# Optimization experiments

Measured on AMD Instinct MI355X. Metric: run time of the kernel, lower is better.

Reference implementation:

```python
import jax, jax.numpy as jnp
import numpy as np

N_NODES = 100000
N_EDGES = 3200000
IN_DIM = 128
OUT_DIM = 128


def setup_inputs() -> dict:
    key = jax.random.key(0)
    k1, k2, k3, k4 = jax.random.split(key, 4)
    features = jax.random.normal(k1, (N_NODES, IN_DIM), dtype=jnp.float32)
    edge_src = jax.random.randint(k2, (N_EDGES,), 0, N_NODES, dtype=jnp.int32)
    edge_dst = jax.random.randint(k3, (N_EDGES,), 0, N_NODES, dtype=jnp.int32)
    # xavier_uniform with relu gain for linear.weight [out_dim, in_dim]
    gain = float(np.sqrt(2.0))  # relu gain
    limit = gain * np.sqrt(6.0 / (IN_DIM + OUT_DIM))
    W = jax.random.uniform(k4, (OUT_DIM, IN_DIM), dtype=jnp.float32,
                           minval=-limit, maxval=limit)
    return {"features": features, "W": W,
            "edge_src": edge_src, "edge_dst": edge_dst}


def reference(features, W, edge_src, edge_dst):
    # in-degrees of each node (messages flow src -> dst), clamp min 1
    degs = jax.ops.segment_sum(jnp.ones_like(edge_dst, dtype=jnp.float32),
                               edge_dst, num_segments=N_NODES)
    norm = jax.lax.rsqrt(jnp.maximum(degs, 1.0))[:, None]  # [N, 1]
    h = features * norm                                    # pre-norm D^-1/2
    # gather messages from src, scatter-sum into dst (edge weight = 1)
    agg = jax.ops.segment_sum(jnp.take(h, edge_src, axis=0), edge_dst,
                              num_segments=N_NODES)        # [N, in_dim]
    h = agg * norm                                         # post-norm D^-1/2
    h = h @ W.T                                            # linear (no bias)
    h = jax.nn.relu(h)                                     # activation
    h = h + features                                       # residual (Identity)
    return h
```

## Files before the change

### kernel.cpp

```cpp
#include <hip/hip_runtime.h>
#include <hip/hip_fp16.h>
#include <hip/hip_fp8.h>

#define N_NODES 100000
#define N_EDGES 3200000
#define DIM 128
#define NB 1000
#define NPB 100
#define CAP 3840
#define SBIN 32

typedef _Float16 f16;
typedef f16 f16x8 __attribute__((ext_vector_type(8)));
typedef float f32x4 __attribute__((ext_vector_type(4)));
typedef float f32x2 __attribute__((ext_vector_type(2)));

__device__ __forceinline__ int bucket_of(int dst) {
    return (int)(((unsigned long long)(unsigned)dst * 42949673ull) >> 32);
}

__device__ __forceinline__ unsigned char f32_to_fp8(float x) {
#if __has_builtin(__builtin_amdgcn_cvt_pk_fp8_f32)
    int r = __builtin_amdgcn_cvt_pk_fp8_f32(x, x, 0, false);
    return (unsigned char)(r & 0xff);
#else
    __hip_fp8_e4m3 q(x);
    return (unsigned char)q.__x;
#endif
}
__device__ __forceinline__ void fp8x4_acc(unsigned u, float& a0, float& a1,
                                          float& a2, float& a3) {
#if __has_builtin(__builtin_amdgcn_cvt_pk_f32_fp8)
    f32x2 lo = __builtin_amdgcn_cvt_pk_f32_fp8((int)u, false);
    f32x2 hi = __builtin_amdgcn_cvt_pk_f32_fp8((int)u, true);
    a0 += lo[0]; a1 += lo[1]; a2 += hi[0]; a3 += hi[1];
#else
    __hip_fp8_e4m3 q0, q1, q2, q3;
    q0.__x = (unsigned char)(u & 0xffu);
    q1.__x = (unsigned char)((u >> 8) & 0xffu);
    q2.__x = (unsigned char)((u >> 16) & 0xffu);
    q3.__x = (unsigned char)((u >> 24) & 0xffu);
    a0 += (float)q0; a1 += (float)q1; a2 += (float)q2; a3 += (float)q3;
#endif
}

__global__ void __launch_bounds__(256) a0_hist(const int* __restrict__ dst,
                                               int* __restrict__ ghist) {
    __shared__ int h[NB];
    for (int i = threadIdx.x; i < NB; i += 256) h[i] = 0;
    __syncthreads();
    const int base = blockIdx.x * 4096 + threadIdx.x;
    #pragma unroll
    for (int i = 0; i < 16; ++i) {
        int e = base + i * 256;
        if (e < N_EDGES) atomicAdd(&h[bucket_of(dst[e])], 1);
    }
    __syncthreads();
    for (int i = threadIdx.x; i < NB; i += 256)
        if (h[i]) atomicAdd(&ghist[i], h[i]);
}

__global__ void __launch_bounds__(1024) bscan_kernel(const int* __restrict__ ghist,
                                                     int* __restrict__ base,
                                                     int* __restrict__ cursor) {
    __shared__ int buf[1024];
    const int v = (threadIdx.x < NB) ? ghist[threadIdx.x] : 0;
    buf[threadIdx.x] = v;
    __syncthreads();
    for (int off = 1; off < 1024; off <<= 1) {
        int t = (threadIdx.x >= off) ? buf[threadIdx.x - off] : 0;
        __syncthreads();
        buf[threadIdx.x] += t;
        __syncthreads();
    }
    if (threadIdx.x < NB) {
        int excl = buf[threadIdx.x] - v;
        base[threadIdx.x] = excl;
        cursor[threadIdx.x] = excl;
    }
    if (threadIdx.x == NB - 1) base[NB] = buf[threadIdx.x];
}

#define A1_CHUNK 16384
#define A1_BLK 1024
#define A1_ITER (A1_CHUNK / A1_BLK)
__global__ void __launch_bounds__(A1_BLK) a1_fill(const int* __restrict__ src,
                                                  const int* __restrict__ dst,
                                                  int* __restrict__ cursor,
                                                  unsigned* __restrict__ ebuf,
                                                  const int fixed) {
    __shared__ int h[NB], off[NB], rk[NB];
    const int tid = threadIdx.x;
    for (int i = tid; i < NB; i += A1_BLK) { h[i] = 0; rk[i] = 0; }
    __syncthreads();
    const int cbase = blockIdx.x * A1_CHUNK;
    int dc[A1_ITER];
    #pragma unroll
    for (int j = 0; j < A1_ITER; ++j) {
        int e = cbase + j * A1_BLK + tid;
        int d = (e < N_EDGES) ? dst[e] : -1;
        dc[j] = d;
        if (d >= 0) atomicAdd(&h[bucket_of(d)], 1);
    }
    __syncthreads();
    for (int i = tid; i < NB; i += A1_BLK) {
        int c = h[i];
        int o = c ? atomicAdd(&cursor[i], c) : 0;
        off[i] = (fixed ? i * CAP : 0) + o;
    }
    __syncthreads();
    #pragma unroll
    for (int j = 0; j < A1_ITER; ++j) {
        int d = dc[j];
        if (d >= 0) {
            int e = cbase + j * A1_BLK + tid;
            int b = bucket_of(d);
            int r = atomicAdd(&rk[b], 1);
            int slot = off[b] + r;
            if (!fixed || slot < (b + 1) * CAP)
                ebuf[slot] = ((unsigned)src[e] << 7) | (unsigned)(d - b * NPB);
        }
    }
}

#define B1_BLK 512
__global__ void __launch_bounds__(B1_BLK) b1_sort(const unsigned* __restrict__ ebuf,
                                                  const int* __restrict__ base,
                                                  const int* __restrict__ cnts,
                                                  const int fixed,
                                                  int* __restrict__ csr,
                                                  int* __restrict__ row_beg,
                                                  int* __restrict__ row_end,
                                                  float* __restrict__ norm) {
    __shared__ int hist[NPB * SBIN], cur[NPB * SBIN], psum[B1_BLK];
    __shared__ int sorted[CAP];
    const int b = blockIdx.x, tid = threadIdx.x;
    int beg, cnt;
    if (fixed) { beg = b * CAP; cnt = min(cnts[b], CAP); }
    else       { beg = base[b]; cnt = base[b + 1] - beg; }
    const int end = beg + cnt;
    for (int i = tid; i < NPB * SBIN; i += B1_BLK) { hist[i] = 0; cur[i] = 0; }
    __syncthreads();
    for (int i = beg + tid; i < end; i += B1_BLK) {
        unsigned w = ebuf[i];
        int key = (int)(w & 127u) * SBIN + (int)(w >> 19);
        atomicAdd(&hist[key], 1);
    }
    __syncthreads();
    {
        int s = 0;
        const int c0 = tid * 7;
        #pragma unroll
        for (int j = 0; j < 7; ++j) {
            int idx = c0 + j;
            if (idx < NPB * SBIN) { int hh = hist[idx]; hist[idx] = s; s += hh; }
        }
        psum[tid] = s;
    }
    __syncthreads();
    for (int off = 1; off < B1_BLK; off <<= 1) {
        int t = (tid >= off) ? psum[tid - off] : 0;
        __syncthreads();
        psum[tid] += t;
        __syncthreads();
    }
    {
        int add = (tid > 0) ? psum[tid - 1] : 0;
        const int c0 = tid * 7;
        #pragma unroll
        for (int j = 0; j < 7; ++j) {
            int idx = c0 + j;
            if (idx < NPB * SBIN) hist[idx] += add;
        }
    }
    __syncthreads();
    if (tid < NPB) {
        int st = hist[tid * SBIN];
        int nx = (tid == NPB - 1) ? cnt : hist[(tid + 1) * SBIN];
        row_beg[b * NPB + tid] = beg + st;
        row_end[b * NPB + tid] = beg + nx;
        norm[b * NPB + tid] = rsqrtf(fmaxf((float)(nx - st), 1.0f));
    }
    __syncthreads();
    if (cnt <= CAP) {
        for (int i = beg + tid; i < end; i += B1_BLK) {
            unsigned w = ebuf[i];
            int s = (int)(w >> 7);
            int key = (int)(w & 127u) * SBIN + (s >> 12);
            int r = atomicAdd(&cur[key], 1);
            sorted[hist[key] + r] = s;
        }
        __syncthreads();
        for (int i = tid; i < cnt; i += B1_BLK) csr[beg + i] = sorted[i];
    } else {
        for (int i = beg + tid; i < end; i += B1_BLK) {
            unsigned w = ebuf[i];
            int s = (int)(w >> 7);
            int key = (int)(w & 127u) * SBIN + (s >> 12);
            int r = atomicAdd(&cur[key], 1);
            csr[beg + hist[key] + r] = s;
        }
    }
}

#define PG_NBLK 512
#define PG_NTILE ((N_NODES + 63) / 64)
__global__ void __launch_bounds__(256, 2) pregemm_mfma(const float* __restrict__ feat,
                                                       const float* __restrict__ W,
                                                       const float* __restrict__ norm,
                                                       unsigned char* __restrict__ g8) {
    const int wid = threadIdx.x >> 6;
    const int l   = threadIdx.x & 63;
    const int lr  = l & 15;
    const int lk  = (l >> 4) * 8;

    f16x8 bf[8][4];
    #pragma unroll
    for (int nt = 0; nt < 8; ++nt) {
        #pragma unroll
        for (int kb = 0; kb < 4; ++kb) {
            const float* wp = W + (size_t)(nt * 16 + lr) * DIM + kb * 32 + lk;
            float4 w0 = *reinterpret_cast<const float4*>(wp);
            float4 w1 = *reinterpret_cast<const float4*>(wp + 4);
            f16x8 t;
            t[0] = (f16)w0.x; t[1] = (f16)w0.y; t[2] = (f16)w0.z; t[3] = (f16)w0.w;
            t[4] = (f16)w1.x; t[5] = (f16)w1.y; t[6] = (f16)w1.z; t[7] = (f16)w1.w;
            bf[nt][kb] = t;
        }
    }

    for (int tile = blockIdx.x; tile < PG_NTILE; tile += PG_NBLK) {
        const int r0 = tile * 64 + wid * 16;
        if (r0 >= N_NODES) continue;
        f32x4 acc[8] = {};
        #pragma unroll
        for (int kb = 0; kb < 4; ++kb) {
            int ar = r0 + lr;
            if (ar >= N_NODES) ar = N_NODES - 1;
            const float* ap = feat + (size_t)ar * DIM + kb * 32 + lk;
            float4 a0 = *reinterpret_cast<const float4*>(ap);
            float4 a1 = *reinterpret_cast<const float4*>(ap + 4);
            f16x8 a;
            a[0] = (f16)a0.x; a[1] = (f16)a0.y; a[2] = (f16)a0.z; a[3] = (f16)a0.w;
            a[4] = (f16)a1.x; a[5] = (f16)a1.y; a[6] = (f16)a1.z; a[7] = (f16)a1.w;
            #pragma unroll
            for (int nt = 0; nt < 8; ++nt)
                acc[nt] = __builtin_amdgcn_mfma_f32_16x16x32_f16(a, bf[nt][kb], acc[nt], 0, 0, 0);
        }
        const int orow0 = r0 + (l >> 4) * 4;
        float nrm[4];
        #pragma unroll
        for (int j = 0; j < 4; ++j)
            nrm[j] = (orow0 + j < N_NODES) ? norm[orow0 + j] : 0.f;
        #pragma unroll
        for (int nt = 0; nt < 8; ++nt) {
            #pragma unroll
            for (int j = 0; j < 4; ++j) {
                int row = orow0 + j;
                if (row < N_NODES)
                    g8[(size_t)row * DIM + nt * 16 + lr] =
                        f32_to_fp8(acc[nt][j] * nrm[j]);
            }
        }
    }
}

#define G2_NBLK (N_NODES / 4)
__global__ void __launch_bounds__(256) gather2(const unsigned char* __restrict__ g8,
                                               const float* __restrict__ norm,
                                               const float* __restrict__ feat,
                                               const int* __restrict__ row_beg,
                                               const int* __restrict__ row_end,
                                               const int* __restrict__ csr,
                                               float* __restrict__ out) {
    const int bswz = (blockIdx.x & 7) * (G2_NBLK / 8) + (blockIdx.x >> 3);
    const int n = bswz * 4 + (threadIdx.x >> 6);
    const int l = threadIdx.x & 63;
    const int sub = l >> 5, li = l & 31;
    const int beg = row_beg[n];
    const int end = row_end[n];
    float a0 = 0.f, a1 = 0.f, a2 = 0.f, a3 = 0.f;
    int e = beg;
    for (; e + 15 < end; e += 16) {
        int s[8];
        #pragma unroll
        for (int j = 0; j < 8; ++j) s[j] = csr[e + 2 * j + sub];
        unsigned u[8];
        #pragma unroll
        for (int j = 0; j < 8; ++j)
            u[j] = reinterpret_cast<const unsigned*>(g8 + (size_t)s[j] * DIM)[li];
        #pragma unroll
        for (int j = 0; j < 8; ++j) fp8x4_acc(u[j], a0, a1, a2, a3);
    }
    for (; e + 7 < end; e += 8) {
        int s[4];
        #pragma unroll
        for (int j = 0; j < 4; ++j) s[j] = csr[e + 2 * j + sub];
        unsigned u[4];
        #pragma unroll
        for (int j = 0; j < 4; ++j)
            u[j] = reinterpret_cast<const unsigned*>(g8 + (size_t)s[j] * DIM)[li];
        #pragma unroll
        for (int j = 0; j < 4; ++j) fp8x4_acc(u[j], a0, a1, a2, a3);
    }
    for (; e + 1 < end; e += 2) {
        const int s = csr[e + sub];
        unsigned u = reinterpret_cast<const unsigned*>(g8 + (size_t)s * DIM)[li];
        fp8x4_acc(u, a0, a1, a2, a3);
    }
    if (e < end) {
        const int s = csr[e];
        unsigned u = reinterpret_cast<const unsigned*>(g8 + (size_t)s * DIM)[li];
        if (sub == 0) fp8x4_acc(u, a0, a1, a2, a3);
    }
    a0 += __shfl_xor(a0, 32);
    a1 += __shfl_xor(a1, 32);
    a2 += __shfl_xor(a2, 32);
    a3 += __shfl_xor(a3, 32);
    if (sub == 0) {
        const float nm = norm[n];
        const float4 f = reinterpret_cast<const float4*>(feat + (size_t)n * DIM)[li];
        float4 o;
        o.x = fmaxf(a0 * nm, 0.f) + f.x;
        o.y = fmaxf(a1 * nm, 0.f) + f.y;
        o.z = fmaxf(a2 * nm, 0.f) + f.z;
        o.w = fmaxf(a3 * nm, 0.f) + f.w;
        reinterpret_cast<float4*>(out + (size_t)n * DIM)[li] = o;
    }
}

#define SCAN_B 1024
#define N_SCANB ((N_NODES + SCAN_B - 1) / SCAN_B)

__global__ void __launch_bounds__(256) deg_kernel(const int* __restrict__ dst,
                                                  int* __restrict__ deg) {
    int i = blockIdx.x * 256 + threadIdx.x;
    if (i < N_EDGES) atomicAdd(&deg[dst[i]], 1);
}
__global__ void __launch_bounds__(SCAN_B) scan1_kernel(const int* __restrict__ deg,
                                                       int* __restrict__ excl,
                                                       int* __restrict__ partials) {
    __shared__ int buf[SCAN_B];
    const int gid = blockIdx.x * SCAN_B + threadIdx.x;
    const int v = (gid < N_NODES) ? deg[gid] : 0;
    buf[threadIdx.x] = v;
    __syncthreads();
    #pragma unroll
    for (int off = 1; off < SCAN_B; off <<= 1) {
        int t = (threadIdx.x >= off) ? buf[threadIdx.x - off] : 0;
        __syncthreads();
        buf[threadIdx.x] += t;
        __syncthreads();
    }
    if (gid < N_NODES) excl[gid] = buf[threadIdx.x] - v;
    if (threadIdx.x == SCAN_B - 1) partials[blockIdx.x] = buf[threadIdx.x];
}
__global__ void __launch_bounds__(128) scan2_kernel(int* __restrict__ partials) {
    __shared__ int buf[128];
    const int v = (threadIdx.x < N_SCANB) ? partials[threadIdx.x] : 0;
    buf[threadIdx.x] = v;
    __syncthreads();
    #pragma unroll
    for (int off = 1; off < 128; off <<= 1) {
        int t = (threadIdx.x >= off) ? buf[threadIdx.x - off] : 0;
        __syncthreads();
        buf[threadIdx.x] += t;
        __syncthreads();
    }
    if (threadIdx.x < N_SCANB) partials[threadIdx.x] = buf[threadIdx.x] - v;
}
__global__ void __launch_bounds__(SCAN_B) scan3_kernel(
        const int* __restrict__ excl, const int* __restrict__ partials,
        const int* __restrict__ deg,
        int* __restrict__ row_start, int* __restrict__ cursor,
        float* __restrict__ norm) {
    const int gid = blockIdx.x * SCAN_B + threadIdx.x;
    if (gid < N_NODES) {
        const int rs = excl[gid] + partials[blockIdx.x];
        row_start[gid] = rs;
        cursor[gid] = rs;
        norm[gid] = rsqrtf(fmaxf((float)deg[gid], 1.0f));
    }
    if (gid == 0) row_start[N_NODES] = N_EDGES;
}
__global__ void __launch_bounds__(256) fill_kernel(
        const int* __restrict__ src, const int* __restrict__ dst,
        int* __restrict__ cursor, int* __restrict__ csr) {
    int i = blockIdx.x * 256 + threadIdx.x;
    if (i < N_EDGES) {
        int pos = atomicAdd(&cursor[dst[i]], 1);
        csr[pos] = src[i];
    }
}
__global__ void __launch_bounds__(256) gather_kernel(
        const float* __restrict__ feat, const float* __restrict__ norm,
        const int* __restrict__ row_start, const int* __restrict__ csr,
        float* __restrict__ out) {
    const int n = blockIdx.x * 4 + (threadIdx.x >> 6);
    if (n >= N_NODES) return;
    const int lane = threadIdx.x & 63;
    const int beg = row_start[n];
    const int end = row_start[n + 1];
    float2 acc = make_float2(0.f, 0.f);
    int e = beg;
    for (; e + 1 < end; e += 2) {
        const int s0 = csr[e], s1 = csr[e + 1];
        const float w0 = norm[s0], w1 = norm[s1];
        const float2 v0 = reinterpret_cast<const float2*>(feat + (size_t)s0 * DIM)[lane];
        const float2 v1 = reinterpret_cast<const float2*>(feat + (size_t)s1 * DIM)[lane];
        acc.x = fmaf(v0.x, w0, acc.x); acc.y = fmaf(v0.y, w0, acc.y);
        acc.x = fmaf(v1.x, w1, acc.x); acc.y = fmaf(v1.y, w1, acc.y);
    }
    if (e < end) {
        const int s0 = csr[e];
        const float w0 = norm[s0];
        const float2 v0 = reinterpret_cast<const float2*>(feat + (size_t)s0 * DIM)[lane];
        acc.x = fmaf(v0.x, w0, acc.x); acc.y = fmaf(v0.y, w0, acc.y);
    }
    reinterpret_cast<float2*>(out + (size_t)n * DIM)[lane] = acc;
}
__global__ void __launch_bounds__(256) final_kernel(
        const float* __restrict__ feat, const float* __restrict__ W,
        const float* __restrict__ norm, float* __restrict__ out) {
    __shared__ float Wt[DIM * DIM];
    __shared__ float rowbuf[8][DIM];
    for (int idx = threadIdx.x; idx < DIM * DIM; idx += 256)
        Wt[idx] = W[(idx & 127) * DIM + (idx >> 7)];
    const int o  = threadIdx.x & 127;
    const int r0 = (threadIdx.x >> 7) * 4;
    for (int rb = blockIdx.x * 8; rb < N_NODES; rb += gridDim.x * 8) {
        __syncthreads();
        float4 v = reinterpret_cast<const float4*>(out + (size_t)rb * DIM)[threadIdx.x];
        reinterpret_cast<float4*>(&rowbuf[0][0])[threadIdx.x] = v;
        __syncthreads();
        float acc0 = 0.f, acc1 = 0.f, acc2 = 0.f, acc3 = 0.f;
        #pragma unroll 8
        for (int k = 0; k < DIM; ++k) {
            float w = Wt[k * DIM + o];
            acc0 = fmaf(rowbuf[r0 + 0][k], w, acc0);
            acc1 = fmaf(rowbuf[r0 + 1][k], w, acc1);
            acc2 = fmaf(rowbuf[r0 + 2][k], w, acc2);
            acc3 = fmaf(rowbuf[r0 + 3][k], w, acc3);
        }
        float accs[4] = {acc0, acc1, acc2, acc3};
        #pragma unroll
        for (int r = 0; r < 4; ++r) {
            int row = rb + r0 + r;
            float val = fmaxf(accs[r] * norm[row], 0.0f) + feat[(size_t)row * DIM + o];
            out[(size_t)row * DIM + o] = val;
        }
    }
}

extern "C" void kernel_launch(void* const* d_in, const int* in_sizes, int n_in,
                              void* d_out, int out_size, void* d_ws, size_t ws_size,
                              hipStream_t stream) {
    const float* feat = (const float*)d_in[0];
    const float* W    = (const float*)d_in[1];
    const int*   src  = (const int*)d_in[2];
    const int*   dst  = (const int*)d_in[3];
    float* out = (float*)d_out;

    const size_t G8_BYTES   = (size_t)N_NODES * DIM;
    const size_t EBUF_FIX   = (size_t)NB * CAP * 4;
    const size_t EBUF_EXACT = (size_t)N_EDGES * 4;
    const int    A1_GRID    = (N_EDGES + A1_CHUNK - 1) / A1_CHUNK;

    {
        char* p = (char*)d_ws;
        unsigned char* g8 = (unsigned char*)p;
        unsigned* ebuf  = (unsigned*)p; p += (G8_BYTES > EBUF_FIX ? G8_BYTES : EBUF_FIX);
        int*      csr   = (int*)p;      p += EBUF_FIX;
        float*    norm  = (float*)p;    p += (size_t)N_NODES * 4;
        int*   row_beg  = (int*)p;      p += (size_t)N_NODES * 4;
        int*   row_end  = (int*)p;      p += (size_t)N_NODES * 4;
        int*   cursor   = (int*)p;      p += NB * 4;
        if (ws_size >= (size_t)(p - (char*)d_ws)) {
            hipMemsetAsync(cursor, 0, NB * sizeof(int), stream);
            a1_fill     <<<A1_GRID, A1_BLK, 0, stream>>>(src, dst, cursor, ebuf, 1);
            b1_sort     <<<NB, B1_BLK, 0, stream>>>(ebuf, nullptr, cursor, 1, csr, row_beg, row_end, norm);
            pregemm_mfma<<<PG_NBLK, 256, 0, stream>>>(feat, W, norm, g8);
            gather2     <<<G2_NBLK, 256, 0, stream>>>(g8, norm, feat, row_beg, row_end, csr, out);
            return;
        }
    }

    {
        char* p = (char*)d_ws;
        unsigned char* g8 = (unsigned char*)p;
        unsigned* ebuf  = (unsigned*)p; p += (G8_BYTES > EBUF_EXACT ? G8_BYTES : EBUF_EXACT);
        int*      csr   = (int*)p;      p += EBUF_EXACT;
        float*    norm  = (float*)p;    p += (size_t)N_NODES * 4;
        int*   row_beg  = (int*)p;      p += (size_t)N_NODES * 4;
        int*   row_end  = (int*)p;      p += (size_t)N_NODES * 4;
        int*      ghist = (int*)p;      p += NB * 4;
        int*      bbase = (int*)p;      p += (NB + 4) * 4;
        int*      bcur  = (int*)p;      p += NB * 4;
        if (ws_size >= (size_t)(p - (char*)d_ws)) {
            hipMemsetAsync(ghist, 0, NB * sizeof(int), stream);
            a0_hist     <<<(N_EDGES + 4095) / 4096, 256, 0, stream>>>(dst, ghist);
            bscan_kernel<<<1, 1024, 0, stream>>>(ghist, bbase, bcur);
            a1_fill     <<<A1_GRID, A1_BLK, 0, stream>>>(src, dst, bcur, ebuf, 0);
            b1_sort     <<<NB, B1_BLK, 0, stream>>>(ebuf, bbase, nullptr, 0, csr, row_beg, row_end, norm);
            pregemm_mfma<<<PG_NBLK, 256, 0, stream>>>(feat, W, norm, g8);
            gather2     <<<G2_NBLK, 256, 0, stream>>>(g8, norm, feat, row_beg, row_end, csr, out);
            return;
        }
    }

    {
        char* q = (char*)d_ws;
        int*   deg       = (int*)q;   q += N_NODES * sizeof(int);
        int*   excl      = (int*)q;   q += N_NODES * sizeof(int);
        int*   cursor    = (int*)q;   q += N_NODES * sizeof(int);
        int*   row_start2= (int*)q;   q += (N_NODES + 1) * sizeof(int);
        float* nrm       = (float*)q; q += N_NODES * sizeof(float);
        int*   partials  = (int*)q;   q += 128 * sizeof(int);
        int*   csr2      = (int*)q;

        hipMemsetAsync(deg, 0, (size_t)N_NODES * sizeof(int), stream);
        deg_kernel  <<<N_EDGES / 256, 256, 0, stream>>>(dst, deg);
        scan1_kernel<<<N_SCANB, SCAN_B, 0, stream>>>(deg, excl, partials);
        scan2_kernel<<<1, 128, 0, stream>>>(partials);
        scan3_kernel<<<N_SCANB, SCAN_B, 0, stream>>>(excl, partials, deg,
                                                     row_start2, cursor, nrm);
        fill_kernel <<<N_EDGES / 256, 256, 0, stream>>>(src, dst, cursor, csr2);
        gather_kernel<<<(N_NODES + 3) / 4, 256, 0, stream>>>(feat, nrm, row_start2, csr2, out);
        final_kernel<<<512, 256, 0, stream>>>(feat, W, nrm, out);
    }
}
```

Measured before the change: 163.2 us.

## Stage bucketed edges in shared memory before coalesced global scatter in a1_fill

The edge-binning kernel now first places each packed edge into a block-local shared-memory buffer ordered by bucket, using a local prefix scan over the bucket histogram. A second pass walks the staged buffer linearly, binary-searches each element's bucket, and writes it to the global bucket region, so consecutive threads write consecutive global addresses within a bucket rather than scattering. The chunk size is halved so the 32 KB staging buffer fits alongside the other shared arrays. This adds a block-wide scan, extra barriers, a per-element binary search and twice as many blocks, hence twice as many global cursor atomics.

```diff
diff --git a/kernel.cpp b/kernel.cpp
--- a/kernel.cpp
+++ b/kernel.cpp
@@ -81,7 +81,7 @@
     if (threadIdx.x == NB - 1) base[NB] = buf[threadIdx.x];
 }
 
-#define A1_CHUNK 16384
+#define A1_CHUNK 8192
 #define A1_BLK 1024
 #define A1_ITER (A1_CHUNK / A1_BLK)
 __global__ void __launch_bounds__(A1_BLK) a1_fill(const int* __restrict__ src,
@@ -89,9 +89,14 @@
                                                   int* __restrict__ cursor,
                                                   unsigned* __restrict__ ebuf,
                                                   const int fixed) {
-    __shared__ int h[NB], off[NB], rk[NB];
+    __shared__ unsigned eloc[A1_CHUNK];
+    __shared__ int h[NB];
+    __shared__ int lexcl[NB + 1];
+    __shared__ int off[NB];
+    __shared__ int psum[A1_BLK];
+    __shared__ int stot;
     const int tid = threadIdx.x;
-    for (int i = tid; i < NB; i += A1_BLK) { h[i] = 0; rk[i] = 0; }
+    for (int i = tid; i < NB; i += A1_BLK) h[i] = 0;
     __syncthreads();
     const int cbase = blockIdx.x * A1_CHUNK;
     int dc[A1_ITER];
@@ -103,11 +108,27 @@
         if (d >= 0) atomicAdd(&h[bucket_of(d)], 1);
     }
     __syncthreads();
+    {
+        int v = (tid < NB) ? h[tid] : 0;
+        psum[tid] = v;
+        __syncthreads();
+        for (int o = 1; o < A1_BLK; o <<= 1) {
+            int t = (tid >= o) ? psum[tid - o] : 0;
+            __syncthreads();
+            psum[tid] += t;
+            __syncthreads();
+        }
+        if (tid < NB) lexcl[tid] = psum[tid] - v;
+        if (tid == 0) { stot = psum[A1_BLK - 1]; lexcl[NB] = psum[A1_BLK - 1]; }
+    }
+    __syncthreads();
     for (int i = tid; i < NB; i += A1_BLK) {
         int c = h[i];
         int o = c ? atomicAdd(&cursor[i], c) : 0;
         off[i] = (fixed ? i * CAP : 0) + o;
     }
+    __syncthreads();
+    for (int i = tid; i < NB; i += A1_BLK) h[i] = 0;
     __syncthreads();
     #pragma unroll
     for (int j = 0; j < A1_ITER; ++j) {
@@ -115,11 +136,24 @@
         if (d >= 0) {
             int e = cbase + j * A1_BLK + tid;
             int b = bucket_of(d);
-            int r = atomicAdd(&rk[b], 1);
-            int slot = off[b] + r;
-            if (!fixed || slot < (b + 1) * CAP)
-                ebuf[slot] = ((unsigned)src[e] << 7) | (unsigned)(d - b * NPB);
-        }
+            int r = atomicAdd(&h[b], 1);
+            eloc[lexcl[b] + r] = ((unsigned)src[e] << 7) | (unsigned)(d - b * NPB);
+        }
+    }
+    __syncthreads();
+    const int total = stot;
+    for (int i = tid; i < total; i += A1_BLK) {
+        unsigned w = eloc[i];
+        int lo = 0, hi = NB;
+        #pragma unroll
+        for (int s = 0; s < 10; ++s) {
+            int mid = (lo + hi + 1) >> 1;
+            if (mid <= NB && lexcl[mid] <= i) lo = mid; else hi = mid - 1;
+        }
+        int b = lo;
+        int gdst = off[b] + (i - lexcl[b]);
+        if (!fixed || gdst < (b + 1) * CAP)
+            ebuf[gdst] = w;
     }
 }
 
```

New measurement: 160.1 us. No clear change (-1.9%).
